# Kernel tuning notes

Hardware: AMD Instinct MI355X
Metric: run time of the kernel (lower is better)

Reference implementation:

```python
import jax, jax.numpy as jnp
import numpy as np

B, C, N, K = 2, 128, 8192, 16
EPS = 1e-5
SLOPE = 0.2


def _knn_idx(coords, k):
    # coords: [B, 3, N] -> idx: [B, N, k] (k nearest neighbors, self excluded)
    pts = jnp.transpose(coords, (0, 2, 1))            # [B, N, 3]
    sq = jnp.sum(pts * pts, axis=-1)                  # [B, N]
    d2 = sq[:, :, None] + sq[:, None, :] - 2.0 * jnp.einsum('bnd,bmd->bnm', pts, pts)
    _, idx = jax.lax.top_k(-d2, k + 1)                # nearest first; first is self (dist 0)
    return idx[:, :, 1:]


def _graph_feature(feats, idx):
    # feats: [B, C, N], idx: [B, N, k] -> [B, 2C, N, k] = concat(center, neighbor - center)
    gather = jax.vmap(lambda f, i: f[:, i])           # [C,N],[N,k] -> [C,N,k]
    neigh = gather(feats, idx)                        # [B, C, N, k]
    center = jnp.broadcast_to(feats[..., None], neigh.shape)
    return jnp.concatenate([center, neigh - center], axis=1)


def _inorm(x):
    # InstanceNorm2d, affine=False: normalize per (b, c) over spatial dims
    m = jnp.mean(x, axis=(2, 3), keepdims=True)
    v = jnp.var(x, axis=(2, 3), keepdims=True)
    return (x - m) * jax.lax.rsqrt(v + EPS)


def _block(x, W):
    # 1x1 conv (no bias) + instance norm + leaky relu
    y = jnp.einsum('oc,bcnk->bonk', W, x)
    return jax.nn.leaky_relu(_inorm(y), SLOPE)


def setup_inputs() -> dict:
    key = jax.random.key(0)
    k0, k1, k2, k3, k4 = jax.random.split(key, 5)
    coords = jax.random.normal(k0, (B, 3, N), dtype=jnp.float32)
    features = jax.random.normal(k1, (B, C, N), dtype=jnp.float32)
    W1 = jax.random.normal(k2, (C, 2 * C), dtype=jnp.float32) * 0.05
    W2 = jax.random.normal(k3, (2 * C, 2 * C), dtype=jnp.float32) * 0.05
    W3 = jax.random.normal(k4, (C, 4 * C), dtype=jnp.float32) * 0.05
    return {"coords": coords, "features": features, "W1": W1, "W2": W2, "W3": W3}


def reference(coords, features, W1, W2, W3):
    idx = _knn_idx(coords, K)                  # same coords for both gathers -> compute once
    x0 = features                              # [B, C, N]
    x1 = _block(_graph_feature(x0, idx), W1).max(axis=-1)   # [B, C, N]
    x2 = _block(_graph_feature(x1, idx), W2).max(axis=-1)   # [B, 2C, N]
    x3 = jnp.concatenate([x0, x1, x2], axis=1)              # [B, 4C, N]
    y = jnp.einsum('oc,bcn->bon', W3, x3)[..., None]        # [B, C, N, 1]
    out = jax.nn.leaky_relu(_inorm(y), SLOPE)[..., 0]       # [B, C, N]
    return out
```

## Files before the change

### kernel.cpp

```cpp
#include <hip/hip_runtime.h>
#include <math.h>

#define NB 2
#define NPTS 8192
#define CH 128
#define KNN 16
#define K17 17
#define EPSI 1e-5f
#define SLOPE 0.2f
#define NCH 32
#define CHSZ 256
#define SCAP 16
#define BIGF 3.0e38f

#define OFF_IDX   0L
#define OFF_X0B   1048576L
#define OFF_YM1   9437184L
#define OFF_YM2   17825792L
#define OFF_UV    34603008L
#define OFF_Y4    68157440L
#define OFF_SURV  OFF_X0B
#define OFF_PA    OFF_Y4
#define OFF_CNT   76546048L
#define OFF_TAU   78643200L
#define OFF_WM1   78708736L
#define OFF_WM2   78839808L
#define OFF_STATS 79101952L
#define OFF_SCB1  79110144L
#define OFF_SCB2  79112192L
#define OFF_PTS4  79116288L


__global__ void zero_stats_k(float* __restrict__ stats) {
  int t = blockIdx.x * 256 + threadIdx.x;
  if (t < 2048) stats[t] = 0.f;
}

__global__ void transpose_x0_k(const float* __restrict__ feat, float* __restrict__ x0b) {
  __shared__ float tile[32][33];
  int b = blockIdx.z;
  int n0 = blockIdx.x * 32, c0 = blockIdx.y * 32;
  int tx = threadIdx.x;
  for (int ty = threadIdx.y; ty < 32; ty += 8)
    tile[ty][tx] = feat[((long)b * CH + c0 + ty) * NPTS + n0 + tx];
  __syncthreads();
  for (int ty = threadIdx.y; ty < 32; ty += 8)
    x0b[((long)b * NPTS + n0 + ty) * 128 + c0 + tx] = tile[tx][ty];
}

__global__ void prep_w_k(const float* __restrict__ W1, const float* __restrict__ W2,
                         float* __restrict__ Wm1, float* __restrict__ Wm2) {
  int t = blockIdx.x * 256 + threadIdx.x;
  if (t < 256 * 128) {
    int r = t >> 7, k = t & 127;
    Wm1[t] = (r < 128) ? (W1[r * 256 + k] - W1[r * 256 + 128 + k])
                       : W1[(r - 128) * 256 + 128 + k];
  }
  if (t < 512 * 128) {
    int r = t >> 7, k = t & 127;
    Wm2[t] = (r < 256) ? (W2[r * 256 + k] - W2[r * 256 + 128 + k])
                       : W2[(r - 256) * 256 + 128 + k];
  }
}

__global__ void finalize_scb_k(const float* __restrict__ stats, float2* __restrict__ scb,
                               int count, float cinv) {
  int t = blockIdx.x * 256 + threadIdx.x;
  if (t < count) {
    float mean = stats[t * 2] * cinv;
    float var = stats[t * 2 + 1] * cinv - mean * mean;
    float inv = rsqrtf(var + EPSI);
    scb[t] = make_float2(inv, -mean * inv);
  }
}

__global__ void knn_prep_k(const float* __restrict__ coords, float4* __restrict__ pts) {
  int b = blockIdx.y;
  int i = blockIdx.x * 256 + threadIdx.x;
  const float* cb = coords + (long)b * 3 * NPTS;
  float x = cb[i], y = cb[NPTS + i], z = cb[2 * NPTS + i];
  float sq = __fadd_rn(__fadd_rn(__fmul_rn(x, x), __fmul_rn(y, y)), __fmul_rn(z, z));
  pts[(long)b * NPTS + i] = make_float4(x, y, z, sq);
}

#define DIST(pi, pj, d2)                                                          \
  float dot = __fadd_rn(__fadd_rn(__fmul_rn((pi).x, (pj).x), __fmul_rn((pi).y, (pj).y)), \
                        __fmul_rn((pi).z, (pj).z));                               \
  float d2 = __fsub_rn(__fadd_rn((pi).w, (pj).w), __fmul_rn(2.0f, dot));

#define KNN_INSERT(d2v, jv)                                              \
  if ((d2v) < d[K17 - 1]) {                                              \
    _Pragma("unroll")                                                    \
    for (int s = K17 - 1; s > 0; --s) {                                  \
      if ((d2v) < d[s - 1]) { d[s] = d[s - 1]; id[s] = id[s - 1]; }      \
      else if ((d2v) < d[s]) { d[s] = (d2v); id[s] = (jv); }             \
    }                                                                    \
    if ((d2v) < d[0]) { d[0] = (d2v); id[0] = (jv); }                    \
  }

__global__ __launch_bounds__(256) void knn_phaseA_k(const float4* __restrict__ pts,
                                                    float2* __restrict__ pa) {
  int b = blockIdx.y;
  int ib = blockIdx.x & 127;
  int sg = blockIdx.x >> 7;
  int i = ib * 64 + (threadIdx.x & 63);
  int sub = sg * 4 + (threadIdx.x >> 6);
  const float4* P = pts + (long)b * NPTS;
  float4 pi = P[i];
  float d0 = BIGF, d1 = BIGF;
  int i0 = 0x7fffffff, i1 = 0x7fffffff;
  int j0 = sub * 64;
  for (int jj = 0; jj < 64; ++jj) {
    float4 pj = P[j0 + jj];
    DIST(pi, pj, d2)
    if (d2 < d1) {
      if (d2 < d0) { d1 = d0; i1 = i0; d0 = d2; i0 = j0 + jj; }
      else { d1 = d2; i1 = j0 + jj; }
    }
  }
  long base = (((long)b * NPTS + i) * 32 + sub) * 2;
  pa[base] = make_float2(d0, __int_as_float(i0));
  pa[base + 1] = make_float2(d1, __int_as_float(i1));
}

__global__ __launch_bounds__(256) void knn_mergeA_k(const float2* __restrict__ pa,
                                                    float* __restrict__ tau) {
  int b = blockIdx.y;
  int i = blockIdx.x * 256 + threadIdx.x;
  float d[K17]; int id[K17];
#pragma unroll
  for (int s = 0; s < K17; ++s) { d[s] = BIGF; id[s] = 0x7fffffff; }
  long base = ((long)b * NPTS + i) * 64;
  for (int c = 0; c < 64; ++c) {
    float2 v = pa[base + c];
    if (v.x < d[K17 - 1]) {
      int j = __float_as_int(v.y);
      KNN_INSERT(v.x, j);
    }
  }
  tau[(long)b * NPTS + i] = d[K17 - 1];
}

__global__ __launch_bounds__(256) void knn_filter_k(const float4* __restrict__ pts,
                                                    const float* __restrict__ tau,
                                                    float2* __restrict__ surv,
                                                    int* __restrict__ counts) {
  int b = blockIdx.z;
  int i = blockIdx.x * 256 + threadIdx.x;
  int chunk = blockIdx.y;
  const float4* P = pts + (long)b * NPTS;
  float4 pi = P[i];
  float t = tau[(long)b * NPTS + i];
  long sbase = (((long)b * NPTS + i) * NCH + chunk) * SCAP;
  int cnt = 0;
  int j0 = chunk * CHSZ;
#pragma unroll 2
  for (int jj = 0; jj < CHSZ; ++jj) {
    float4 pj = P[j0 + jj];
    DIST(pi, pj, d2)
    if (d2 <= t) {
      if (cnt < SCAP) surv[sbase + cnt] = make_float2(d2, __int_as_float(j0 + jj));
      cnt++;
    }
  }
  counts[((long)b * NPTS + i) * NCH + chunk] = cnt;
}

__global__ __launch_bounds__(256) void knn_mergeB_k(const float2* __restrict__ surv,
                                                    const int* __restrict__ counts,
                                                    const float4* __restrict__ pts,
                                                    int* __restrict__ idxo) {
  __shared__ float2 lds[8][K17][32];
  int b = blockIdx.y;
  int pl = threadIdx.x & 31;
  int sub = threadIdx.x >> 5;
  int i = blockIdx.x * 32 + pl;
  const float4* P = pts + (long)b * NPTS;
  float4 pi = P[i];
  float d[K17]; int id[K17];
#pragma unroll
  for (int s = 0; s < K17; ++s) { d[s] = BIGF; id[s] = 0x7fffffff; }
  long cbase = ((long)b * NPTS + i) * NCH;
  int4 c4 = *(const int4*)(counts + cbase + sub * 4);
  int cnt4[4] = {c4.x, c4.y, c4.z, c4.w};
#pragma unroll
  for (int q = 0; q < 4; ++q) {
    int c = sub * 4 + q;
    int cnt = cnt4[q];
    if (cnt > SCAP) {
      int j0 = c * CHSZ;
      for (int jj = 0; jj < CHSZ; ++jj) {
        float4 pj = P[j0 + jj];
        DIST(pi, pj, d2)
        KNN_INSERT(d2, j0 + jj);
      }
    } else {
      long sb = (cbase + c) * SCAP;
      for (int p = 0; p < cnt; p += 2) {
        float4 v2 = *(const float4*)(surv + sb + p);
        if (v2.x < d[K17 - 1]) {
          int j = __float_as_int(v2.y);
          KNN_INSERT(v2.x, j);
        }
        if (p + 1 < cnt && v2.z < d[K17 - 1]) {
          int j = __float_as_int(v2.w);
          KNN_INSERT(v2.z, j);
        }
      }
    }
  }
#pragma unroll
  for (int s = 0; s < K17; ++s) lds[sub][s][pl] = make_float2(d[s], __int_as_float(id[s]));
  __syncthreads();
  if ((sub & 1) == 0) {
#pragma unroll
    for (int s = 0; s < K17; ++s) {
      float2 v = lds[sub + 1][s][pl];
      if (v.x < d[K17 - 1]) {
        int j = __float_as_int(v.y);
        KNN_INSERT(v.x, j);
      }
    }
  }
  __syncthreads();
  if ((sub & 1) == 0) {
#pragma unroll
    for (int s = 0; s < K17; ++s) lds[sub >> 1][s][pl] = make_float2(d[s], __int_as_float(id[s]));
  }
  __syncthreads();
  if (sub < 2) {
#pragma unroll
    for (int s = 0; s < K17; ++s) {
      float2 v = lds[2 * sub][s][pl];
      d[s] = v.x; id[s] = __float_as_int(v.y);
    }
#pragma unroll
    for (int s = 0; s < K17; ++s) {
      float2 v = lds[2 * sub + 1][s][pl];
      if (v.x < d[K17 - 1]) {
        int j = __float_as_int(v.y);
        KNN_INSERT(v.x, j);
      }
    }
  }
  __syncthreads();
  if (sub < 2) {
#pragma unroll
    for (int s = 0; s < K17; ++s) lds[sub][s][pl] = make_float2(d[s], __int_as_float(id[s]));
  }
  __syncthreads();
  if (sub == 0) {
#pragma unroll
    for (int s = 0; s < K17; ++s) {
      float2 v = lds[0][s][pl];
      d[s] = v.x; id[s] = __float_as_int(v.y);
    }
#pragma unroll
    for (int s = 0; s < K17; ++s) {
      float2 v = lds[1][s][pl];
      if (v.x < d[K17 - 1]) {
        int j = __float_as_int(v.y);
        KNN_INSERT(v.x, j);
      }
    }
    long ob = ((long)b * NPTS + i) * KNN;
#pragma unroll
    for (int s = 1; s < K17; ++s) idxo[ob + s - 1] = id[s];
  }
}

#define GBN 128
#define GBM 64
#define GBK 32
__global__ __launch_bounds__(256) void gemm_xt_k(const float* __restrict__ X, int sx, long xbs,
                                                 const float* __restrict__ W, int K,
                                                 float* __restrict__ Out, int so, long obs) {
  __shared__ float Xs[GBK][GBN + 4];
  __shared__ float Ws[GBK][GBM + 4];
  int b = blockIdx.z;
  const float* Xb = X + (long)b * xbs;
  float* Ob = Out + (long)b * obs;
  int n0 = blockIdx.x * GBN, m0 = blockIdx.y * GBM;
  int tx = threadIdx.x, ty = threadIdx.y;
  int tid = ty * 16 + tx;
  float acc[8][4];
#pragma unroll
  for (int i = 0; i < 8; ++i)
#pragma unroll
    for (int j = 0; j < 4; ++j) acc[i][j] = 0.f;

  for (int k0 = 0; k0 < K; k0 += GBK) {
#pragma unroll
    for (int i = 0; i < 4; ++i) {
      int q = tid + i * 256;
      int r = q >> 3, kq = (q & 7) * 4;
      const float4 v = *(const float4*)(Xb + (long)(n0 + r) * sx + k0 + kq);
      Xs[kq][r] = v.x; Xs[kq + 1][r] = v.y; Xs[kq + 2][r] = v.z; Xs[kq + 3][r] = v.w;
    }
#pragma unroll
    for (int i = 0; i < 2; ++i) {
      int q = tid + i * 256;
      int r = q >> 3, kq = (q & 7) * 4;
      const float4 v = *(const float4*)(W + (long)(m0 + r) * K + k0 + kq);
      Ws[kq][r] = v.x; Ws[kq + 1][r] = v.y; Ws[kq + 2][r] = v.z; Ws[kq + 3][r] = v.w;
    }
    __syncthreads();
#pragma unroll
    for (int kk = 0; kk < GBK; ++kk) {
      float4 w4 = *(const float4*)&Ws[kk][tx * 4];
      float4 xa = *(const float4*)&Xs[kk][ty * 8];
      float4 xb4 = *(const float4*)&Xs[kk][ty * 8 + 4];
      float xs[8] = {xa.x, xa.y, xa.z, xa.w, xb4.x, xb4.y, xb4.z, xb4.w};
      float wv[4] = {w4.x, w4.y, w4.z, w4.w};
#pragma unroll
      for (int i = 0; i < 8; ++i)
#pragma unroll
        for (int j = 0; j < 4; ++j) acc[i][j] = fmaf(xs[i], wv[j], acc[i][j]);
    }
    __syncthreads();
  }
#pragma unroll
  for (int i = 0; i < 8; ++i) {
    float4 v = make_float4(acc[i][0], acc[i][1], acc[i][2], acc[i][3]);
    *(float4*)(Ob + (long)(n0 + ty * 8 + i) * so + m0 + tx * 4) = v;
  }
}

#define AFFLK4(v, a0, a1, a2, a3)                              \
  v.x = fmaf(v.x, a0.x, a0.y); v.x = fmaxf(v.x, SLOPE * v.x);  \
  v.y = fmaf(v.y, a1.x, a1.y); v.y = fmaxf(v.y, SLOPE * v.y);  \
  v.z = fmaf(v.z, a2.x, a2.y); v.z = fmaxf(v.z, SLOPE * v.z);  \
  v.w = fmaf(v.w, a3.x, a3.y); v.w = fmaxf(v.w, SLOPE * v.w);

__global__ __launch_bounds__(256) void gemm_aff_k(const float* __restrict__ X,
                                                  const float2* __restrict__ scb,
                                                  const float* __restrict__ W,
                                                  float* __restrict__ Out, int so, long obs) {
  __shared__ float Xs[GBK][GBN + 4];
  __shared__ float Ws[GBK][GBM + 4];
  int b = blockIdx.z;
  const float* Xb = X + (long)b * NPTS * 128;
  const float2* sc = scb + b * 128;
  float* Ob = Out + (long)b * obs;
  int n0 = blockIdx.x * GBN, m0 = blockIdx.y * GBM;
  int tx = threadIdx.x, ty = threadIdx.y;
  int tid = ty * 16 + tx;
  float acc[8][4];
#pragma unroll
  for (int i = 0; i < 8; ++i)
#pragma unroll
    for (int j = 0; j < 4; ++j) acc[i][j] = 0.f;

  for (int k0 = 0; k0 < 128; k0 += GBK) {
#pragma unroll
    for (int i = 0; i < 4; ++i) {
      int q = tid + i * 256;
      int r = q >> 3, kq = (q & 7) * 4;
      float4 v = *(const float4*)(Xb + (long)(n0 + r) * 128 + k0 + kq);
      float2 a0 = sc[k0 + kq], a1 = sc[k0 + kq + 1], a2 = sc[k0 + kq + 2], a3 = sc[k0 + kq + 3];
      AFFLK4(v, a0, a1, a2, a3)
      Xs[kq][r] = v.x; Xs[kq + 1][r] = v.y; Xs[kq + 2][r] = v.z; Xs[kq + 3][r] = v.w;
    }
#pragma unroll
    for (int i = 0; i < 2; ++i) {
      int q = tid + i * 256;
      int r = q >> 3, kq = (q & 7) * 4;
      const float4 v = *(const float4*)(W + (long)(m0 + r) * 128 + k0 + kq);
      Ws[kq][r] = v.x; Ws[kq + 1][r] = v.y; Ws[kq + 2][r] = v.z; Ws[kq + 3][r] = v.w;
    }
    __syncthreads();
#pragma unroll
    for (int kk = 0; kk < GBK; ++kk) {
      float4 w4 = *(const float4*)&Ws[kk][tx * 4];
      float4 xa = *(const float4*)&Xs[kk][ty * 8];
      float4 xb4 = *(const float4*)&Xs[kk][ty * 8 + 4];
      float xs[8] = {xa.x, xa.y, xa.z, xa.w, xb4.x, xb4.y, xb4.z, xb4.w};
      float wv[4] = {w4.x, w4.y, w4.z, w4.w};
#pragma unroll
      for (int i = 0; i < 8; ++i)
#pragma unroll
        for (int j = 0; j < 4; ++j) acc[i][j] = fmaf(xs[i], wv[j], acc[i][j]);
    }
    __syncthreads();
  }
#pragma unroll
  for (int i = 0; i < 8; ++i) {
    float4 v = make_float4(acc[i][0], acc[i][1], acc[i][2], acc[i][3]);
    *(float4*)(Ob + (long)(n0 + ty * 8 + i) * so + m0 + tx * 4) = v;
  }
}

__global__ __launch_bounds__(256) void gemm_cat_k(const float* __restrict__ x0b,
                                                  const float* __restrict__ ym1,
                                                  const float* __restrict__ ym2,
                                                  const float2* __restrict__ scb1,
                                                  const float2* __restrict__ scb2,
                                                  const float* __restrict__ W,
                                                  float* __restrict__ Out,
                                                  float* __restrict__ st4) {
  __shared__ float Xs[GBK][GBN + 4];
  __shared__ float Ws[GBK][GBM + 4];
  int b = blockIdx.z;
  float* Ob = Out + (long)b * NPTS * 128;
  int n0 = blockIdx.x * GBN, m0 = blockIdx.y * GBM;
  int tx = threadIdx.x, ty = threadIdx.y;
  int tid = ty * 16 + tx;
  float acc[8][4];
#pragma unroll
  for (int i = 0; i < 8; ++i)
#pragma unroll
    for (int j = 0; j < 4; ++j) acc[i][j] = 0.f;

  for (int k0 = 0; k0 < 512; k0 += GBK) {
    const float* Xb; long st_; const float2* sc_; int cb_;
    if (k0 < 128)      { Xb = x0b + (long)b * NPTS * 128; st_ = 128; sc_ = nullptr;        cb_ = 0; }
    else if (k0 < 256) { Xb = ym1 + (long)b * NPTS * 128; st_ = 128; sc_ = scb1 + b * 128; cb_ = 128; }
    else               { Xb = ym2 + (long)b * NPTS * 256; st_ = 256; sc_ = scb2 + b * 256; cb_ = 256; }
    int kl = k0 - cb_;
#pragma unroll
    for (int i = 0; i < 4; ++i) {
      int q = tid + i * 256;
      int r = q >> 3, kq = (q & 7) * 4;
      float4 v = *(const float4*)(Xb + (long)(n0 + r) * st_ + kl + kq);
      if (sc_) {
        float2 a0 = sc_[kl + kq], a1 = sc_[kl + kq + 1], a2 = sc_[kl + kq + 2], a3 = sc_[kl + kq + 3];
        AFFLK4(v, a0, a1, a2, a3)
      }
      Xs[kq][r] = v.x; Xs[kq + 1][r] = v.y; Xs[kq + 2][r] = v.z; Xs[kq + 3][r] = v.w;
    }
#pragma unroll
    for (int i = 0; i < 2; ++i) {
      int q = tid + i * 256;
      int r = q >> 3, kq = (q & 7) * 4;
      const float4 v = *(const float4*)(W + (long)(m0 + r) * 512 + k0 + kq);
      Ws[kq][r] = v.x; Ws[kq + 1][r] = v.y; Ws[kq + 2][r] = v.z; Ws[kq + 3][r] = v.w;
    }
    __syncthreads();
#pragma unroll
    for (int kk = 0; kk < GBK; ++kk) {
      float4 w4 = *(const float4*)&Ws[kk][tx * 4];
      float4 xa = *(const float4*)&Xs[kk][ty * 8];
      float4 xb4 = *(const float4*)&Xs[kk][ty * 8 + 4];
      float xs[8] = {xa.x, xa.y, xa.z, xa.w, xb4.x, xb4.y, xb4.z, xb4.w};
      float wv[4] = {w4.x, w4.y, w4.z, w4.w};
#pragma unroll
      for (int i = 0; i < 8; ++i)
#pragma unroll
        for (int j = 0; j < 4; ++j) acc[i][j] = fmaf(xs[i], wv[j], acc[i][j]);
    }
    __syncthreads();
  }
#pragma unroll
  for (int i = 0; i < 8; ++i) {
    float4 v = make_float4(acc[i][0], acc[i][1], acc[i][2], acc[i][3]);
    *(float4*)(Ob + (long)(n0 + ty * 8 + i) * 128 + m0 + tx * 4) = v;
  }
  float cs[4] = {0.f, 0.f, 0.f, 0.f}, cq[4] = {0.f, 0.f, 0.f, 0.f};
#pragma unroll
  for (int i = 0; i < 8; ++i)
#pragma unroll
    for (int j = 0; j < 4; ++j) { cs[j] += acc[i][j]; cq[j] = fmaf(acc[i][j], acc[i][j], cq[j]); }
  float* red = (float*)Xs;
  int base = (tx * 16 + ty) * 8;
#pragma unroll
  for (int j = 0; j < 4; ++j) { red[base + 2 * j] = cs[j]; red[base + 2 * j + 1] = cq[j]; }
  __syncthreads();
  if (ty == 0) {
#pragma unroll
    for (int yy = 1; yy < 16; ++yy) {
      int bb = (tx * 16 + yy) * 8;
#pragma unroll
      for (int j = 0; j < 4; ++j) { cs[j] += red[bb + 2 * j]; cq[j] += red[bb + 2 * j + 1]; }
    }
    float* st = st4 + ((long)b * 128 + m0 + tx * 4) * 2;
#pragma unroll
    for (int j = 0; j < 4; ++j) {
      atomicAdd(&st[2 * j], cs[j]);
      atomicAdd(&st[2 * j + 1], cq[j]);
    }
  }
}

template <int CTILE, int PPB>
__global__ __launch_bounds__(256) void edge_max_t(const float* __restrict__ uv, int S, int voff,
                                                  int Cout, const int* __restrict__ idx,
                                                  float* __restrict__ ymax,
                                                  float* __restrict__ stats) {
  constexpr int CG = CTILE / 4;
  constexpr int PSL = 256 / CG;
  __shared__ float ls[2][256][4];
  int blk = blockIdx.x;
  int c = (blk & 7) >> 1;
  int b = c >> 1;
  int ct = c & 1;
  int pblk = ((blk >> 3) << 1) | (blk & 1);
  int ch0 = ct * CTILE;
  const float* uvb = uv + (long)b * NPTS * S;
  const int* idxb = idx + (long)b * NPTS * KNN;
  float* ymb = ymax + (long)b * NPTS * Cout;
  int cg = threadIdx.x & (CG - 1);
  int ps = threadIdx.x / CG;
  int n0 = pblk * PPB;
  const float* vb = uvb + voff + ch0 + 4 * cg;
  float4 s = make_float4(0.f, 0.f, 0.f, 0.f);
  float4 s2 = make_float4(0.f, 0.f, 0.f, 0.f);
  for (int p = ps; p < PPB; p += PSL) {
    int n = n0 + p;
    const int* ip = idxb + n * KNN;
    int4 ia = *(const int4*)(ip);
    int4 ib4 = *(const int4*)(ip + 4);
    int4 ic = *(const int4*)(ip + 8);
    int4 id4 = *(const int4*)(ip + 12);
    int mi[KNN] = {ia.x, ia.y, ia.z, ia.w, ib4.x, ib4.y, ib4.z, ib4.w,
                   ic.x, ic.y, ic.z, ic.w, id4.x, id4.y, id4.z, id4.w};
    float4 u = *(const float4*)(uvb + (long)n * S + ch0 + 4 * cg);
    float4 mx = make_float4(-INFINITY, -INFINITY, -INFINITY, -INFINITY);
#pragma unroll
    for (int k = 0; k < KNN; ++k) {
      float4 v = *(const float4*)(vb + (long)mi[k] * S);
      float4 y;
      y.x = u.x + v.x; y.y = u.y + v.y; y.z = u.z + v.z; y.w = u.w + v.w;
      mx.x = fmaxf(mx.x, y.x); mx.y = fmaxf(mx.y, y.y);
      mx.z = fmaxf(mx.z, y.z); mx.w = fmaxf(mx.w, y.w);
      s.x += y.x; s.y += y.y; s.z += y.z; s.w += y.w;
      s2.x = fmaf(y.x, y.x, s2.x); s2.y = fmaf(y.y, y.y, s2.y);
      s2.z = fmaf(y.z, y.z, s2.z); s2.w = fmaf(y.w, y.w, s2.w);
    }
    *(float4*)(ymb + (long)n * Cout + ch0 + 4 * cg) = mx;
  }
  int t = threadIdx.x;
  ls[0][t][0] = s.x; ls[0][t][1] = s.y; ls[0][t][2] = s.z; ls[0][t][3] = s.w;
  ls[1][t][0] = s2.x; ls[1][t][1] = s2.y; ls[1][t][2] = s2.z; ls[1][t][3] = s2.w;
  __syncthreads();
  if (ps == 0) {
#pragma unroll
    for (int j = 1; j < PSL; ++j) {
      int q = j * CG + cg;
      s.x += ls[0][q][0]; s.y += ls[0][q][1]; s.z += ls[0][q][2]; s.w += ls[0][q][3];
      s2.x += ls[1][q][0]; s2.y += ls[1][q][1]; s2.z += ls[1][q][2]; s2.w += ls[1][q][3];
    }
    float* st = stats + ((long)b * Cout + ch0 + 4 * cg) * 2;
    atomicAdd(&st[0], s.x); atomicAdd(&st[1], s2.x);
    atomicAdd(&st[2], s.y); atomicAdd(&st[3], s2.y);
    atomicAdd(&st[4], s.z); atomicAdd(&st[5], s2.z);
    atomicAdd(&st[6], s.w); atomicAdd(&st[7], s2.w);
  }
}

__global__ void final_k(const float* __restrict__ y3, const float* __restrict__ stats,
                        float* __restrict__ out) {
  __shared__ float tile[32][33];
  int b = blockIdx.z;
  int n0 = blockIdx.x * 32, o0 = blockIdx.y * 32;
  int tx = threadIdx.x;
  for (int ty = threadIdx.y; ty < 32; ty += 8) {
    int o = o0 + tx;
    const float* st = stats + ((long)b * 128 + o) * 2;
    float mean = st[0] * (1.f / 8192.f);
    float var = st[1] * (1.f / 8192.f) - mean * mean;
    float inv = rsqrtf(var + EPSI);
    float y = y3[((long)b * NPTS + n0 + ty) * 128 + o];
    float z = (y - mean) * inv;
    tile[ty][tx] = z >= 0.f ? z : SLOPE * z;
  }
  __syncthreads();
  for (int ty = threadIdx.y; ty < 32; ty += 8)
    out[((long)b * CH + o0 + ty) * NPTS + n0 + tx] = tile[tx][ty];
}

extern "C" void kernel_launch(void* const* d_in, const int* in_sizes, int n_in,
                              void* d_out, int out_size, void* d_ws, size_t ws_size,
                              hipStream_t stream) {
  const float* coords = (const float*)d_in[0];
  const float* features = (const float*)d_in[1];
  const float* W1 = (const float*)d_in[2];
  const float* W2 = (const float*)d_in[3];
  const float* W3 = (const float*)d_in[4];
  float* out = (float*)d_out;
  char* ws = (char*)d_ws;

  int* idx = (int*)(ws + OFF_IDX);
  float* x0b = (float*)(ws + OFF_X0B);
  float* ym1 = (float*)(ws + OFF_YM1);
  float* ym2 = (float*)(ws + OFF_YM2);
  float* uv = (float*)(ws + OFF_UV);
  float* y4 = (float*)(ws + OFF_Y4);
  float2* surv = (float2*)(ws + OFF_SURV);
  float2* pa = (float2*)(ws + OFF_PA);
  int* counts = (int*)(ws + OFF_CNT);
  float* tau = (float*)(ws + OFF_TAU);
  float* wm1 = (float*)(ws + OFF_WM1);
  float* wm2 = (float*)(ws + OFF_WM2);
  float* stats = (float*)(ws + OFF_STATS);
  float2* scb1 = (float2*)(ws + OFF_SCB1);
  float2* scb2 = (float2*)(ws + OFF_SCB2);
  float4* pts4 = (float4*)(ws + OFF_PTS4);

  zero_stats_k<<<8, 256, 0, stream>>>(stats);
  knn_prep_k<<<dim3(NPTS / 256, NB), 256, 0, stream>>>(coords, pts4);
  knn_phaseA_k<<<dim3(1024, NB), 256, 0, stream>>>(pts4, pa);
  knn_mergeA_k<<<dim3(NPTS / 256, NB), 256, 0, stream>>>(pa, tau);
  knn_filter_k<<<dim3(NPTS / 256, NCH, NB), 256, 0, stream>>>(pts4, tau, surv, counts);
  knn_mergeB_k<<<dim3(NPTS / 32, NB), 256, 0, stream>>>(surv, counts, pts4, idx);

  transpose_x0_k<<<dim3(NPTS / 32, CH / 32, NB), dim3(32, 8), 0, stream>>>(features, x0b);
  prep_w_k<<<256, 256, 0, stream>>>(W1, W2, wm1, wm2);

  gemm_xt_k<<<dim3(NPTS / GBN, 256 / GBM, NB), dim3(16, 16), 0, stream>>>(
      x0b, 128, (long)NPTS * 128, wm1, 128, uv, 256, (long)NPTS * 256);
  edge_max_t<64, 32><<<dim3(NPTS / 32 * 2 * NB), 256, 0, stream>>>(uv, 256, 128, 128, idx,
                                                                   ym1, stats);
  finalize_scb_k<<<1, 256, 0, stream>>>(stats, scb1, 256, 1.0f / 131072.0f);
  gemm_aff_k<<<dim3(NPTS / GBN, 512 / GBM, NB), dim3(16, 16), 0, stream>>>(
      ym1, scb1, wm2, uv, 512, (long)NPTS * 512);
  edge_max_t<128, 32><<<dim3(NPTS / 32 * 2 * NB), 256, 0, stream>>>(uv, 512, 256, 256, idx,
                                                                    ym2, stats + 512);
  finalize_scb_k<<<2, 256, 0, stream>>>(stats + 512, scb2, 512, 1.0f / 131072.0f);
  gemm_cat_k<<<dim3(NPTS / GBN, 128 / GBM, NB), dim3(16, 16), 0, stream>>>(
      x0b, ym1, ym2, scb1, scb2, W3, y4, stats + 1536);
  final_k<<<dim3(NPTS / 32, CH / 32, NB), dim3(32, 8), 0, stream>>>(y4, stats + 1536, out);
}
```

Before: 499.1 us.

## Split final concat GEMM along K into two halves with separate reduce-and-stats kernel

The last 512-deep GEMM is split into two K halves written to separate buffers, doubling the block count for more parallelism. A new kernel sums the two partial outputs in place and accumulates per-channel mean/variance statistics with atomics, replacing the in-GEMM reduction. This adds an extra read/write pass over the output and one more launch in exchange for better occupancy of the GEMM.

```diff
diff --git a/kernel.cpp b/kernel.cpp
--- a/kernel.cpp
+++ b/kernel.cpp
@@ -396,13 +396,15 @@
                                                   const float2* __restrict__ scb1,
                                                   const float2* __restrict__ scb2,
                                                   const float* __restrict__ W,
-                                                  float* __restrict__ Out,
-                                                  float* __restrict__ st4) {
+                                                  float* __restrict__ OutA,
+                                                  float* __restrict__ OutB) {
   __shared__ float Xs[GBK][GBN + 4];
   __shared__ float Ws[GBK][GBM + 4];
   int b = blockIdx.z;
-  float* Ob = Out + (long)b * NPTS * 128;
-  int n0 = blockIdx.x * GBN, m0 = blockIdx.y * GBM;
+  int mt = blockIdx.y & 1;
+  int kh = blockIdx.y >> 1;
+  float* Ob = (kh ? OutB : OutA) + (long)b * NPTS * 128;
+  int n0 = blockIdx.x * GBN, m0 = mt * GBM;
   int tx = threadIdx.x, ty = threadIdx.y;
   int tid = ty * 16 + tx;
   float acc[8][4];
@@ -411,7 +413,8 @@
 #pragma unroll
     for (int j = 0; j < 4; ++j) acc[i][j] = 0.f;
 
-  for (int k0 = 0; k0 < 512; k0 += GBK) {
+  for (int ks = 0; ks < 8; ++ks) {
+    int k0 = kh * 256 + ks * GBK;
     const float* Xb; long st_; const float2* sc_; int cb_;
     if (k0 < 128)      { Xb = x0b + (long)b * NPTS * 128; st_ = 128; sc_ = nullptr;        cb_ = 0; }
     else if (k0 < 256) { Xb = ym1 + (long)b * NPTS * 128; st_ = 128; sc_ = scb1 + b * 128; cb_ = 128; }
@@ -454,30 +457,6 @@
   for (int i = 0; i < 8; ++i) {
     float4 v = make_float4(acc[i][0], acc[i][1], acc[i][2], acc[i][3]);
     *(float4*)(Ob + (long)(n0 + ty * 8 + i) * 128 + m0 + tx * 4) = v;
-  }
-  float cs[4] = {0.f, 0.f, 0.f, 0.f}, cq[4] = {0.f, 0.f, 0.f, 0.f};
-#pragma unroll
-  for (int i = 0; i < 8; ++i)
-#pragma unroll
-    for (int j = 0; j < 4; ++j) { cs[j] += acc[i][j]; cq[j] = fmaf(acc[i][j], acc[i][j], cq[j]); }
-  float* red = (float*)Xs;
-  int base = (tx * 16 + ty) * 8;
-#pragma unroll
-  for (int j = 0; j < 4; ++j) { red[base + 2 * j] = cs[j]; red[base + 2 * j + 1] = cq[j]; }
-  __syncthreads();
-  if (ty == 0) {
-#pragma unroll
-    for (int yy = 1; yy < 16; ++yy) {
-      int bb = (tx * 16 + yy) * 8;
-#pragma unroll
-      for (int j = 0; j < 4; ++j) { cs[j] += red[bb + 2 * j]; cq[j] += red[bb + 2 * j + 1]; }
-    }
-    float* st = st4 + ((long)b * 128 + m0 + tx * 4) * 2;
-#pragma unroll
-    for (int j = 0; j < 4; ++j) {
-      atomicAdd(&st[2 * j], cs[j]);
-      atomicAdd(&st[2 * j + 1], cq[j]);
-    }
   }
 }
 
@@ -547,6 +526,24 @@
   }
 }
 
+__global__ void colstats2_k(float* __restrict__ y4, const float* __restrict__ y4b,
+                            float* __restrict__ stats) {
+  int b = blockIdx.y;
+  int o = threadIdx.x & 127, slot = threadIdx.x >> 7;
+  int n0 = blockIdx.x * 64;
+  float s = 0.f, s2 = 0.f;
+  for (int p = slot; p < 64; p += 2) {
+    long off = ((long)b * NPTS + n0 + p) * 128 + o;
+    float y = y4[off] + y4b[off];
+    y4[off] = y;
+    s += y;
+    s2 = fmaf(y, y, s2);
+  }
+  float* st = stats + ((long)b * 128 + o) * 2;
+  atomicAdd(&st[0], s);
+  atomicAdd(&st[1], s2);
+}
+
 __global__ void final_k(const float* __restrict__ y3, const float* __restrict__ stats,
                         float* __restrict__ out) {
   __shared__ float tile[32][33];
@@ -616,7 +613,8 @@
   edge_max_t<128, 32><<<dim3(NPTS / 32 * 2 * NB), 256, 0, stream>>>(uv, 512, 256, 256, idx,
                                                                     ym2, stats + 512);
   finalize_scb_k<<<2, 256, 0, stream>>>(stats + 512, scb2, 512, 1.0f / 131072.0f);
-  gemm_cat_k<<<dim3(NPTS / GBN, 128 / GBM, NB), dim3(16, 16), 0, stream>>>(
-      x0b, ym1, ym2, scb1, scb2, W3, y4, stats + 1536);
+  gemm_cat_k<<<dim3(NPTS / GBN, 4, NB), dim3(16, 16), 0, stream>>>(
+      x0b, ym1, ym2, scb1, scb2, W3, y4, uv);
+  colstats2_k<<<dim3(NPTS / 64, NB), 256, 0, stream>>>(y4, uv, stats + 1536);
   final_k<<<dim3(NPTS / 32, CH / 32, NB), dim3(32, 8), 0, stream>>>(y4, stats + 1536, out);
 }
```

Result: faster. 487.2 us (-2.4%).
